# Kernel optimization log

Measured on AMD Instinct MI355X. Metric: run time of the kernel, lower is better.

## Reference

```python
import jax, jax.numpy as jnp
import numpy as np

N = 8192
EMB = 256
NHID = 64
ALPHA = 0.2  # LeakyReLU negative slope
NEG_INF = -9e15


def setup_inputs() -> dict:
    key = jax.random.key(0)
    k1, k2, k3, k4 = jax.random.split(key, 4)
    inp = jax.random.normal(k1, (N, EMB), dtype=jnp.float32)
    adj = jax.random.randint(k2, (N, N), 0, 2, dtype=jnp.int32)
    W = jax.random.normal(k3, (EMB, NHID), dtype=jnp.float32) * 0.05
    a = jax.random.normal(k4, (2 * NHID,), dtype=jnp.float32) * 0.05
    return {"input": inp, "adj": adj, "W": W, "a": a}


def reference(input, adj, W, a):
    # h = W(input): [N, nhid]
    h = input @ W
    # e_ij = leakyrelu(h_i . a[:nhid] + h_j . a[nhid:])  (equiv. to concat-pairs @ a)
    s_src = h @ a[:NHID]   # [N]
    s_dst = h @ a[NHID:]   # [N]
    e = jax.nn.leaky_relu(s_src[:, None] + s_dst[None, :], ALPHA)  # [N, N]
    attention = jnp.where(adj > 0, e, NEG_INF)
    attention = jax.nn.softmax(attention, axis=1)
    # edge dropout p=0.0 (eval) -> identity
    h_prime = attention @ h  # [N, nhid]
    return h_prime
```

## Files before the change

### kernel.cpp

```cpp
#include <hip/hip_runtime.h>
#include <hip/hip_bf16.h>

#define N_NODES 8192
#define EMB 256
#define NHID 64
#define LOG2E 1.44269504088896340736f
#define S_SPLIT 8
#define COLS_PER 1024
#define NKT 32

typedef __attribute__((ext_vector_type(8))) short bf16x8;
typedef __attribute__((ext_vector_type(4))) float f32x4;

static __device__ __forceinline__ short f2bf(float f) {
  __hip_bfloat16 h = __float2bfloat16(f);
  return *reinterpret_cast<short*>(&h);
}

static __device__ __forceinline__ short f2bf_fast(float f) {
  unsigned u = __builtin_bit_cast(unsigned, f);
  return (short)((u + 0x8000u) >> 16);
}

__global__ __launch_bounds__(256) void gat_k1(
    const float* __restrict__ in, const float* __restrict__ W,
    const float* __restrict__ a, short* __restrict__ hT,
    float* __restrict__ ssrc, float* __restrict__ sdst) {
  int wave = threadIdx.x >> 6, lane = threadIdx.x & 63;
  int row = blockIdx.x * 4 + wave;
  int d = lane;
  const float4* in4 = reinterpret_cast<const float4*>(in + (size_t)row * EMB);
  float acc = 0.f;
#pragma unroll 4
  for (int k4 = 0; k4 < EMB / 4; ++k4) {
    float4 x = in4[k4];
    int k = k4 * 4;
    acc = fmaf(x.x, W[(k + 0) * NHID + d], acc);
    acc = fmaf(x.y, W[(k + 1) * NHID + d], acc);
    acc = fmaf(x.z, W[(k + 2) * NHID + d], acc);
    acc = fmaf(x.w, W[(k + 3) * NHID + d], acc);
  }
  hT[(size_t)d * N_NODES + row] = f2bf(acc);
  float p1 = acc * a[d];
  float p2 = acc * a[NHID + d];
#pragma unroll
  for (int off = 32; off > 0; off >>= 1) {
    p1 += __shfl_xor(p1, off);
    p2 += __shfl_xor(p2, off);
  }
  if (lane == 0) {
    ssrc[row] = p1 * LOG2E;
    sdst[row] = p2 * LOG2E;
  }
}

__global__ __launch_bounds__(256, 4) void gat_k2(
    const int* __restrict__ adj, const short* __restrict__ hT,
    const float* __restrict__ ssrc, const float* __restrict__ sdst,
    float* __restrict__ pacc, float* __restrict__ pz) {
  int rb = blockIdx.x / S_SPLIT;
  int split = blockIdx.x % S_SPLIT;
  int wv = threadIdx.x >> 6, lane = threadIdx.x & 63;
  int lrow = lane & 15, kg = lane >> 4;
  int r0 = rb * 64 + wv * 16;
  int row = r0 + lrow;
  float s_i = ssrc[row];
  const int* adjr = adj + (size_t)row * N_NODES;
  const short* h0 = hT + (size_t)(0 * 16 + lrow) * N_NODES;
  const short* h1 = hT + (size_t)(1 * 16 + lrow) * N_NODES;
  const short* h2 = hT + (size_t)(2 * 16 + lrow) * N_NODES;
  const short* h3 = hT + (size_t)(3 * 16 + lrow) * N_NODES;
  f32x4 acc0 = {0.f, 0.f, 0.f, 0.f};
  f32x4 acc1 = acc0, acc2 = acc0, acc3 = acc0;
  float zacc = 0.f;
  int jbase = split * COLS_PER + kg * 8;

  int4 aA0 = *reinterpret_cast<const int4*>(adjr + jbase);
  int4 aB0 = *reinterpret_cast<const int4*>(adjr + jbase + 4);
  int4 aA1 = *reinterpret_cast<const int4*>(adjr + jbase + 32);
  int4 aB1 = *reinterpret_cast<const int4*>(adjr + jbase + 36);
  float4 tA = *reinterpret_cast<const float4*>(sdst + jbase);
  float4 tB = *reinterpret_cast<const float4*>(sdst + jbase + 4);

#pragma unroll 2
  for (int kt = 0; kt < NKT; ++kt) {
    int jb = jbase + kt * 32;
    int j2 = jbase + ((kt + 2) & (NKT - 1)) * 32;
    int j1 = jbase + ((kt + 1) & (NKT - 1)) * 32;
    int4 nA = *reinterpret_cast<const int4*>(adjr + j2);
    int4 nB = *reinterpret_cast<const int4*>(adjr + j2 + 4);
    float4 ntA = *reinterpret_cast<const float4*>(sdst + j1);
    float4 ntB = *reinterpret_cast<const float4*>(sdst + j1 + 4);
    bf16x8 b0 = *reinterpret_cast<const bf16x8*>(h0 + jb);
    bf16x8 b1 = *reinterpret_cast<const bf16x8*>(h1 + jb);
    bf16x8 b2 = *reinterpret_cast<const bf16x8*>(h2 + jb);
    bf16x8 b3 = *reinterpret_cast<const bf16x8*>(h3 + jb);

    float tv[8] = {tA.x, tA.y, tA.z, tA.w, tB.x, tB.y, tB.z, tB.w};
    int av[8] = {aA0.x, aA0.y, aA0.z, aA0.w, aB0.x, aB0.y, aB0.z, aB0.w};
    bf16x8 af;
#pragma unroll
    for (int e = 0; e < 8; ++e) {
      float x = s_i + tv[e];
      float lk = fmaxf(x, 0.2f * x);
      float ev = __builtin_amdgcn_exp2f(lk);
      float w = (av[e] != 0) ? ev : 0.f;
      zacc += w;
      af[e] = f2bf_fast(w);
    }
    acc0 = __builtin_amdgcn_mfma_f32_16x16x32_bf16(af, b0, acc0, 0, 0, 0);
    acc1 = __builtin_amdgcn_mfma_f32_16x16x32_bf16(af, b1, acc1, 0, 0, 0);
    acc2 = __builtin_amdgcn_mfma_f32_16x16x32_bf16(af, b2, acc2, 0, 0, 0);
    acc3 = __builtin_amdgcn_mfma_f32_16x16x32_bf16(af, b3, acc3, 0, 0, 0);

    aA0 = aA1; aB0 = aB1; aA1 = nA; aB1 = nB;
    tA = ntA; tB = ntB;
  }

  float z = zacc;
  z += __shfl_xor(z, 16);
  z += __shfl_xor(z, 32);
  if (lane < 16) pz[(size_t)split * N_NODES + r0 + lane] = z;

  float* pa = pacc + (size_t)split * (N_NODES * NHID);
#pragma unroll
  for (int reg = 0; reg < 4; ++reg) {
    int orow = r0 + kg * 4 + reg;
    pa[(size_t)orow * NHID + 0 * 16 + lrow] = acc0[reg];
    pa[(size_t)orow * NHID + 1 * 16 + lrow] = acc1[reg];
    pa[(size_t)orow * NHID + 2 * 16 + lrow] = acc2[reg];
    pa[(size_t)orow * NHID + 3 * 16 + lrow] = acc3[reg];
  }
}

__global__ __launch_bounds__(256) void gat_k3(
    const float* __restrict__ pacc, const float* __restrict__ pz,
    float* __restrict__ out) {
  int idx = blockIdx.x * 256 + threadIdx.x;
  int row = idx >> 6;
  float num = 0.f, den = 0.f;
#pragma unroll
  for (int s = 0; s < S_SPLIT; ++s) {
    num += pacc[(size_t)s * (N_NODES * NHID) + idx];
    den += pz[(size_t)s * N_NODES + row];
  }
  out[idx] = num / den;
}

extern "C" void kernel_launch(void* const* d_in, const int* in_sizes, int n_in,
                              void* d_out, int out_size, void* d_ws, size_t ws_size,
                              hipStream_t stream) {
  (void)in_sizes; (void)n_in; (void)out_size; (void)ws_size;
  const float* in = (const float*)d_in[0];
  const int* adj = (const int*)d_in[1];
  const float* W = (const float*)d_in[2];
  const float* a = (const float*)d_in[3];
  float* out = (float*)d_out;

  char* w = (char*)d_ws;
  short* hT = (short*)w;
  float* ssrc = (float*)(w + (1u << 20));
  float* sdst = ssrc + N_NODES;
  float* pz = sdst + N_NODES;
  float* pacc = pz + (size_t)S_SPLIT * N_NODES;

  gat_k1<<<N_NODES / 4, 256, 0, stream>>>(in, W, a, hT, ssrc, sdst);
  gat_k2<<<(N_NODES / 64) * S_SPLIT, 256, 0, stream>>>(adj, hT, ssrc, sdst,
                                                       pacc, pz);
  gat_k3<<<(N_NODES * NHID) / 256, 256, 0, stream>>>(pacc, pz, out);
}
```

Before: 472.3 us.

## Stage hT column tile and sdst in LDS with a finer column split

The attention-aggregation kernel now copies a 64x256 bf16 slice of hT and the matching sdst values into padded shared memory once per block, then reads MFMA B-operands from LDS instead of global memory. The column split grows from 8 to 32 and blocks are ordered split-major, so blocks running at the same time share the same hT tile. Adjacency loads use a three-deep register prefetch ring, and the loop is fully unrolled. The trade-off is four times more partial-accumulator traffic written by the aggregation kernel and read back in the reduction kernel, plus higher workspace use.

```diff
diff --git a/kernel.cpp b/kernel.cpp
--- a/kernel.cpp
+++ b/kernel.cpp
@@ -5,9 +5,10 @@
 #define EMB 256
 #define NHID 64
 #define LOG2E 1.44269504088896340736f
-#define S_SPLIT 8
-#define COLS_PER 1024
-#define NKT 32
+#define S_SPLIT 32
+#define COLS 256
+#define NKT 8
+#define HROWB 264
 
 typedef __attribute__((ext_vector_type(8))) short bf16x8;
 typedef __attribute__((ext_vector_type(4))) float f32x4;
@@ -58,46 +59,65 @@
     const int* __restrict__ adj, const short* __restrict__ hT,
     const float* __restrict__ ssrc, const float* __restrict__ sdst,
     float* __restrict__ pacc, float* __restrict__ pz) {
-  int rb = blockIdx.x / S_SPLIT;
-  int split = blockIdx.x % S_SPLIT;
-  int wv = threadIdx.x >> 6, lane = threadIdx.x & 63;
+  __shared__ short hlds[64 * HROWB];
+  __shared__ float tlds[COLS];
+
+  int split = blockIdx.x >> 7;
+  int rb = blockIdx.x & 127;
+  int tid = threadIdx.x;
+  int c0 = split * COLS;
+
+#pragma unroll
+  for (int p = 0; p < 8; ++p) {
+    int flat = p * 4096 + tid * 16;
+    int srow = flat >> 9;
+    int scol = (flat & 511) >> 1;
+    bf16x8 v = *reinterpret_cast<const bf16x8*>(
+        hT + (size_t)srow * N_NODES + c0 + scol);
+    *reinterpret_cast<bf16x8*>(&hlds[srow * HROWB + scol]) = v;
+  }
+  if (tid < 64) {
+    float4 tv4 = *reinterpret_cast<const float4*>(sdst + c0 + tid * 4);
+    *reinterpret_cast<float4*>(&tlds[tid * 4]) = tv4;
+  }
+  __syncthreads();
+
+  int wv = tid >> 6, lane = tid & 63;
   int lrow = lane & 15, kg = lane >> 4;
   int r0 = rb * 64 + wv * 16;
   int row = r0 + lrow;
   float s_i = ssrc[row];
-  const int* adjr = adj + (size_t)row * N_NODES;
-  const short* h0 = hT + (size_t)(0 * 16 + lrow) * N_NODES;
-  const short* h1 = hT + (size_t)(1 * 16 + lrow) * N_NODES;
-  const short* h2 = hT + (size_t)(2 * 16 + lrow) * N_NODES;
-  const short* h3 = hT + (size_t)(3 * 16 + lrow) * N_NODES;
+  const int* adjr = adj + (size_t)row * N_NODES + c0 + kg * 8;
+
   f32x4 acc0 = {0.f, 0.f, 0.f, 0.f};
   f32x4 acc1 = acc0, acc2 = acc0, acc3 = acc0;
   float zacc = 0.f;
-  int jbase = split * COLS_PER + kg * 8;
 
-  int4 aA0 = *reinterpret_cast<const int4*>(adjr + jbase);
-  int4 aB0 = *reinterpret_cast<const int4*>(adjr + jbase + 4);
-  int4 aA1 = *reinterpret_cast<const int4*>(adjr + jbase + 32);
-  int4 aB1 = *reinterpret_cast<const int4*>(adjr + jbase + 36);
-  float4 tA = *reinterpret_cast<const float4*>(sdst + jbase);
-  float4 tB = *reinterpret_cast<const float4*>(sdst + jbase + 4);
+  int4 rgA[3], rgB[3];
+#pragma unroll
+  for (int i = 0; i < 3; ++i) {
+    rgA[i] = *reinterpret_cast<const int4*>(adjr + i * 32);
+    rgB[i] = *reinterpret_cast<const int4*>(adjr + i * 32 + 4);
+  }
 
-#pragma unroll 2
+#pragma unroll
   for (int kt = 0; kt < NKT; ++kt) {
-    int jb = jbase + kt * 32;
-    int j2 = jbase + ((kt + 2) & (NKT - 1)) * 32;
-    int j1 = jbase + ((kt + 1) & (NKT - 1)) * 32;
-    int4 nA = *reinterpret_cast<const int4*>(adjr + j2);
-    int4 nB = *reinterpret_cast<const int4*>(adjr + j2 + 4);
-    float4 ntA = *reinterpret_cast<const float4*>(sdst + j1);
-    float4 ntB = *reinterpret_cast<const float4*>(sdst + j1 + 4);
-    bf16x8 b0 = *reinterpret_cast<const bf16x8*>(h0 + jb);
-    bf16x8 b1 = *reinterpret_cast<const bf16x8*>(h1 + jb);
-    bf16x8 b2 = *reinterpret_cast<const bf16x8*>(h2 + jb);
-    bf16x8 b3 = *reinterpret_cast<const bf16x8*>(h3 + jb);
+    int rs = kt % 3;
+    int4 ca = rgA[rs], cb = rgB[rs];
+    if (kt + 3 < NKT) {
+      rgA[rs] = *reinterpret_cast<const int4*>(adjr + (kt + 3) * 32);
+      rgB[rs] = *reinterpret_cast<const int4*>(adjr + (kt + 3) * 32 + 4);
+    }
+    int cbase = kt * 32 + kg * 8;
+    float4 tA = *reinterpret_cast<const float4*>(&tlds[cbase]);
+    float4 tB = *reinterpret_cast<const float4*>(&tlds[cbase + 4]);
+    bf16x8 b0 = *reinterpret_cast<const bf16x8*>(&hlds[(lrow + 0) * HROWB + cbase]);
+    bf16x8 b1 = *reinterpret_cast<const bf16x8*>(&hlds[(lrow + 16) * HROWB + cbase]);
+    bf16x8 b2 = *reinterpret_cast<const bf16x8*>(&hlds[(lrow + 32) * HROWB + cbase]);
+    bf16x8 b3 = *reinterpret_cast<const bf16x8*>(&hlds[(lrow + 48) * HROWB + cbase]);
 
     float tv[8] = {tA.x, tA.y, tA.z, tA.w, tB.x, tB.y, tB.z, tB.w};
-    int av[8] = {aA0.x, aA0.y, aA0.z, aA0.w, aB0.x, aB0.y, aB0.z, aB0.w};
+    int av[8] = {ca.x, ca.y, ca.z, ca.w, cb.x, cb.y, cb.z, cb.w};
     bf16x8 af;
 #pragma unroll
     for (int e = 0; e < 8; ++e) {
@@ -112,9 +132,6 @@
     acc1 = __builtin_amdgcn_mfma_f32_16x16x32_bf16(af, b1, acc1, 0, 0, 0);
     acc2 = __builtin_amdgcn_mfma_f32_16x16x32_bf16(af, b2, acc2, 0, 0, 0);
     acc3 = __builtin_amdgcn_mfma_f32_16x16x32_bf16(af, b3, acc3, 0, 0, 0);
-
-    aA0 = aA1; aB0 = aB1; aA1 = nA; aB1 = nB;
-    tA = ntA; tB = ntB;
   }
 
   float z = zacc;
@@ -139,7 +156,7 @@
   int idx = blockIdx.x * 256 + threadIdx.x;
   int row = idx >> 6;
   float num = 0.f, den = 0.f;
-#pragma unroll
+#pragma unroll 8
   for (int s = 0; s < S_SPLIT; ++s) {
     num += pacc[(size_t)s * (N_NODES * NHID) + idx];
     den += pz[(size_t)s * N_NODES + row];
@@ -165,7 +182,6 @@
   float* pacc = pz + (size_t)S_SPLIT * N_NODES;
 
   gat_k1<<<N_NODES / 4, 256, 0, stream>>>(in, W, a, hT, ssrc, sdst);
-  gat_k2<<<(N_NODES / 64) * S_SPLIT, 256, 0, stream>>>(adj, hT, ssrc, sdst,
-                                                       pacc, pz);
+  gat_k2<<<128 * S_SPLIT, 256, 0, stream>>>(adj, hT, ssrc, sdst, pacc, pz);
   gat_k3<<<(N_NODES * NHID) / 256, 256, 0, stream>>>(pacc, pz, out);
 }
```

Result: faster. 449.0 us (-4.9%).
